# Kernel tuning notes

Measured on AMD Instinct MI355X. Metric: run time of the kernel, lower is better.

The kernel has to match this reference:

```python
import jax, jax.numpy as jnp
import numpy as np

HIDDEN = 1024
NUM_HEADS = 16
HEAD_DIM = HIDDEN // NUM_HEADS


def setup_inputs() -> dict:
    key = jax.random.key(0)
    ks = jax.random.split(key, 5)
    scale = 1.0 / np.sqrt(HIDDEN)
    x = jax.random.normal(ks[0], (2, 2048, HIDDEN), dtype=jnp.float32)
    qkv_w = jax.random.uniform(ks[1], (3 * HIDDEN, HIDDEN), jnp.float32, -scale, scale)
    qkv_b = jax.random.uniform(ks[2], (3 * HIDDEN,), jnp.float32, -scale, scale)
    out_w = jax.random.uniform(ks[3], (HIDDEN, HIDDEN), jnp.float32, -scale, scale)
    out_b = jax.random.uniform(ks[4], (HIDDEN,), jnp.float32, -scale, scale)
    return {"x": x, "qkv_w": qkv_w, "qkv_b": qkv_b, "out_w": out_w, "out_b": out_b}


def reference(x, qkv_w, qkv_b, out_w, out_b):
    B, S, _ = x.shape
    qkv = jnp.einsum('bsd,ed->bse', x, qkv_w) + qkv_b  # [B,S,3H]
    q, k, v = jnp.split(qkv, 3, axis=-1)
    # [B,S,H] -> [B,nh,S,hd]
    def to_heads(t):
        return t.reshape(B, S, NUM_HEADS, HEAD_DIM).transpose(0, 2, 1, 3)
    q, k, v = to_heads(q), to_heads(k), to_heads(v)
    scores = jnp.einsum('bhqd,bhkd->bhqk', q, k) / np.sqrt(HEAD_DIM).astype(np.float32)
    attn = jax.nn.softmax(scores, axis=-1)
    o = jnp.einsum('bhqk,bhkd->bhqd', attn, v)
    o = o.transpose(0, 2, 1, 3).reshape(B, S, HIDDEN)
    return jnp.einsum('bsd,ed->bse', o, out_w) + out_b
```

## Files before the change

### kernel.cpp

```cpp
#include <hip/hip_runtime.h>
#include <stdint.h>

typedef __bf16 bf16x8 __attribute__((ext_vector_type(8)));
typedef float  f32x4  __attribute__((ext_vector_type(4)));
typedef float  f32x16 __attribute__((ext_vector_type(16)));
typedef unsigned short u16;
typedef unsigned int   u32;

#define B_  2
#define S_  2048
#define H_  1024
#define NH_ 16
#define HD_ 64
#define QSCL 0.18033688011112042f

__device__ __forceinline__ u16 f2bf(float f) {
  u32 u = __builtin_bit_cast(u32, f);
  return (u16)((u + 0x7FFFu + ((u >> 16) & 1u)) >> 16);
}
__device__ __forceinline__ float ex2(float x) { return __builtin_amdgcn_exp2f(x); }
__device__ __forceinline__ u32 cvtpk(float lo, float hi) {
  u32 r; asm("v_cvt_pk_bf16_f32 %0, %1, %2" : "=v"(r) : "v"(lo), "v"(hi)); return r;
}
__device__ __forceinline__ void gload_lds16(const u16* g, u16* lds) {
  __builtin_amdgcn_global_load_lds(
      (__attribute__((address_space(1))) void*)(void*)g,
      (__attribute__((address_space(3))) void*)lds, 16, 0, 0);
}

__global__ void cvt_all(const float* __restrict__ a, const float* __restrict__ b,
                        const float* __restrict__ c, u16* __restrict__ oa,
                        u16* __restrict__ ob, u16* __restrict__ oc) {
  int i = blockIdx.x * 256 + threadIdx.x;
  const float4* src; ushort4* dst; int j;
  if (i < 1048576)      { src = (const float4*)a; dst = (ushort4*)oa; j = i; }
  else if (i < 1835008) { src = (const float4*)b; dst = (ushort4*)ob; j = i - 1048576; }
  else                  { src = (const float4*)c; dst = (ushort4*)oc; j = i - 1835008; }
  const float4 v = src[j];
  ushort4 o;
  o.x = f2bf(v.x); o.y = f2bf(v.y); o.z = f2bf(v.z); o.w = f2bf(v.w);
  dst[j] = o;
}

__global__ __launch_bounds__(256, 2)
void gemm_qkv(const u16* __restrict__ A, const u16* __restrict__ W,
              const float* __restrict__ bias,
              u16* __restrict__ qb, u16* __restrict__ kb, u16* __restrict__ vtb,
              int M, int N, int K)
{
  __shared__ __align__(16) u16 As[128 * 32];
  __shared__ __align__(16) u16 Bs[128 * 32];
  const int tid = threadIdx.x;
  const int w = tid >> 6, l = tid & 63;
  const int lg = l >> 4, lr = l & 15;
  const int wr = w >> 1, wc = w & 1;
  const int tM = blockIdx.y * 128, tN = blockIdx.x * 128;

  f32x4 acc[4][4];
  const f32x4 z4 = {0.f, 0.f, 0.f, 0.f};
#pragma unroll
  for (int m = 0; m < 4; ++m)
#pragma unroll
    for (int n = 0; n < 4; ++n) acc[m][n] = z4;

  for (int k0 = 0; k0 < K; k0 += 32) {
    __syncthreads();
#pragma unroll
    for (int i = 0; i < 2; ++i) {
      const int ch = i * 256 + tid;
      const int row = ch >> 2, cc = (ch & 3) * 8;
      gload_lds16(A + (size_t)(tM + row) * K + k0 + cc, As + (size_t)(i * 256 + w * 64) * 8);
      gload_lds16(W + (size_t)(tN + row) * K + k0 + cc, Bs + (size_t)(i * 256 + w * 64) * 8);
    }
    __syncthreads();
    bf16x8 af[4], bw[4];
#pragma unroll
    for (int m = 0; m < 4; ++m)
      af[m] = *(const bf16x8*)&As[(wr * 64 + m * 16 + lr) * 32 + lg * 8];
#pragma unroll
    for (int n = 0; n < 4; ++n)
      bw[n] = *(const bf16x8*)&Bs[(wc * 64 + n * 16 + lr) * 32 + lg * 8];
#pragma unroll
    for (int m = 0; m < 4; ++m)
#pragma unroll
      for (int n = 0; n < 4; ++n)
        acc[m][n] = __builtin_amdgcn_mfma_f32_16x16x32_bf16(af[m], bw[n], acc[m][n], 0, 0, 0);
  }

#pragma unroll
  for (int n = 0; n < 4; ++n) {
    const int col = tN + wc * 64 + n * 16 + lr;
    const float bv = bias[col];
    const int t3 = col >> 10, rem = col & 1023;
    const int hh = rem >> 6, dd = rem & 63;
    const float sc = (t3 == 0) ? QSCL : 1.f;
    u16* dst = (t3 == 0) ? qb : (t3 == 1) ? kb : vtb;
#pragma unroll
    for (int m = 0; m < 4; ++m)
#pragma unroll
      for (int r = 0; r < 4; ++r) {
        const int row = tM + wr * 64 + m * 16 + lg * 4 + r;
        const int bb = row >> 11, ss = row & 2047;
        const u16 val = f2bf((acc[m][n][r] + bv) * sc);
        if (t3 < 2) dst[((size_t)(bb * NH_ + hh) * S_ + ss) * HD_ + dd] = val;
        else        dst[((size_t)(bb * NH_ + hh) * HD_ + dd) * S_ + ss] = val;
      }
  }
}

__global__ __launch_bounds__(256, 2)
void gemm_out(const u16* __restrict__ A, const u16* __restrict__ W,
              const float* __restrict__ bias, float* __restrict__ outf,
              int M, int N, int K)
{
  __shared__ __align__(16) u16 As[128 * 32];
  __shared__ __align__(16) u16 Bs[64 * 32];
  const int tid = threadIdx.x;
  const int w = tid >> 6, l = tid & 63;
  const int lg = l >> 4, lr = l & 15;
  const int tM = blockIdx.y * 128, tN = blockIdx.x * 64;

  f32x4 acc[2][4];
  const f32x4 z4 = {0.f, 0.f, 0.f, 0.f};
#pragma unroll
  for (int m = 0; m < 2; ++m)
#pragma unroll
    for (int n = 0; n < 4; ++n) acc[m][n] = z4;

  for (int k0 = 0; k0 < K; k0 += 32) {
    __syncthreads();
#pragma unroll
    for (int i = 0; i < 2; ++i) {
      const int ch = i * 256 + tid;
      const int row = ch >> 2, cc = (ch & 3) * 8;
      gload_lds16(A + (size_t)(tM + row) * K + k0 + cc, As + (size_t)(i * 256 + w * 64) * 8);
    }
    gload_lds16(W + (size_t)(tN + (tid >> 2)) * K + k0 + (tid & 3) * 8, Bs + (size_t)(w * 64) * 8);
    __syncthreads();
    bf16x8 af[2], bw[4];
#pragma unroll
    for (int m = 0; m < 2; ++m)
      af[m] = *(const bf16x8*)&As[(w * 32 + m * 16 + lr) * 32 + lg * 8];
#pragma unroll
    for (int n = 0; n < 4; ++n)
      bw[n] = *(const bf16x8*)&Bs[(n * 16 + lr) * 32 + lg * 8];
#pragma unroll
    for (int m = 0; m < 2; ++m)
#pragma unroll
      for (int n = 0; n < 4; ++n)
        acc[m][n] = __builtin_amdgcn_mfma_f32_16x16x32_bf16(af[m], bw[n], acc[m][n], 0, 0, 0);
  }

#pragma unroll
  for (int n = 0; n < 4; ++n) {
    const int col = tN + n * 16 + lr;
    const float bv = bias[col];
#pragma unroll
    for (int m = 0; m < 2; ++m)
#pragma unroll
      for (int r = 0; r < 4; ++r) {
        const int row = tM + w * 32 + m * 16 + lg * 4 + r;
        outf[(size_t)row * N + col] = acc[m][n][r] + bv;
      }
  }
}

__global__ __launch_bounds__(256, 2)
void attn_fwd(const u16* __restrict__ qb, const u16* __restrict__ kb,
              const u16* __restrict__ vtb, u16* __restrict__ ob)
{
  __shared__ __align__(16) u16 Kl[2][64 * 64];
  __shared__ __align__(16) u16 Vl[2][64 * 64];

  const int tid = threadIdx.x;
  const int w = tid >> 6, l = tid & 63;
  const int q32 = l & 31, hi = l >> 5;
  const int idx = blockIdx.x;
  const int bh = idx & 31, qt = idx >> 5;
  const int bb = bh >> 4, hh = bh & 15;
  const int q0 = qt * 128 + w * 32;

  bf16x8 qf[4];
#pragma unroll
  for (int ks = 0; ks < 4; ++ks)
    qf[ks] = *(const bf16x8*)&qb[((size_t)bh * S_ + q0 + q32) * HD_ + ks * 16 + hi * 8];

  const f32x16 z16 = {};
  f32x16 acc[2] = {z16, z16};
  float lrun = 0.f;

  const int srow = l >> 3;
  const int scol = ((l & 7) ^ srow) << 3;
  const u16* kbase = kb  + ((size_t)bh * S_  + w * 16 + srow) * HD_ + scol;
  const u16* vbase = vtb + ((size_t)bh * HD_ + w * 16 + srow) * S_  + scol;

  auto STAGE = [&](int buf, int t) {
#pragma unroll
    for (int j = 0; j < 2; ++j) {
      gload_lds16(kbase + (size_t)t * 64 * HD_ + j * 8 * HD_, &Kl[buf][(w * 16 + j * 8) * 64]);
      gload_lds16(vbase + (size_t)t * 64 + j * 8 * S_,        &Vl[buf][(w * 16 + j * 8) * 64]);
    }
  };

  STAGE(0, 0);
  __syncthreads();

  const int sw = q32 & 7;

  for (int t = 0; t < 32; ++t) {
    const int cur = t & 1;
    if (t + 1 < 32) STAGE(cur ^ 1, t + 1);

    f32x16 st[2] = {z16, z16};
    __builtin_amdgcn_s_setprio(1);
#pragma unroll
    for (int kt = 0; kt < 2; ++kt)
#pragma unroll
      for (int ks = 0; ks < 4; ++ks) {
        const bf16x8 kf = *(const bf16x8*)&Kl[cur][(kt * 32 + q32) * 64 + ((((ks << 1) | hi) ^ sw) << 3)];
        st[kt] = __builtin_amdgcn_mfma_f32_32x32x16_bf16(kf, qf[ks], st[kt], 0, 0, 0);
      }
    __builtin_amdgcn_s_setprio(0);

    bf16x8 pa[4];
#pragma unroll
    for (int kt = 0; kt < 2; ++kt) {
      float p[16];
#pragma unroll
      for (int r = 0; r < 16; ++r) p[r] = ex2(st[kt][r]);
#pragma unroll
      for (int g = 0; g < 4; ++g)
        lrun += (p[4 * g] + p[4 * g + 1]) + (p[4 * g + 2] + p[4 * g + 3]);
      u32 wk0[4], wk1[4];
#pragma unroll
      for (int g = 0; g < 4; ++g) {
        wk0[g] = cvtpk(p[4 * g], p[4 * g + 1]);
        wk1[g] = cvtpk(p[4 * g + 2], p[4 * g + 3]);
      }
#pragma unroll
      for (int k2 = 0; k2 < 2; ++k2) {
        u32 a0 = wk0[2 * k2], b0 = wk0[2 * k2 + 1];
        u32 a1 = wk1[2 * k2], b1 = wk1[2 * k2 + 1];
        asm volatile("v_permlane32_swap_b32 %0, %1" : "+v"(a0), "+v"(b0));
        asm volatile("v_permlane32_swap_b32 %0, %1" : "+v"(a1), "+v"(b1));
        uint4 wv = {a0, a1, b0, b1};
        pa[kt * 2 + k2] = __builtin_bit_cast(bf16x8, wv);
      }
    }

    __builtin_amdgcn_s_setprio(1);
#pragma unroll
    for (int dt = 0; dt < 2; ++dt)
#pragma unroll
      for (int ks = 0; ks < 4; ++ks) {
        const bf16x8 vf = *(const bf16x8*)&Vl[cur][(dt * 32 + q32) * 64 + ((((ks << 1) | hi) ^ sw) << 3)];
        acc[dt] = __builtin_amdgcn_mfma_f32_32x32x16_bf16(vf, pa[ks], acc[dt], 0, 0, 0);
      }
    __builtin_amdgcn_s_setprio(0);

    __syncthreads();
  }

  lrun += __shfl_xor(lrun, 32);
  const float linv = 1.f / lrun;
  const size_t orow = ((size_t)(bb * S_ + q0 + q32)) * H_ + hh * HD_;
#pragma unroll
  for (int dt = 0; dt < 2; ++dt)
#pragma unroll
    for (int g = 0; g < 4; ++g) {
      const u32 o0 = cvtpk(acc[dt][4 * g] * linv, acc[dt][4 * g + 1] * linv);
      const u32 o1 = cvtpk(acc[dt][4 * g + 2] * linv, acc[dt][4 * g + 3] * linv);
      uint2 ov; ov.x = o0; ov.y = o1;
      *(uint2*)&ob[orow + dt * 32 + g * 8 + hi * 4] = ov;
    }
}

extern "C" void kernel_launch(void* const* d_in, const int* in_sizes, int n_in,
                              void* d_out, int out_size, void* d_ws, size_t ws_size,
                              hipStream_t stream) {
  const float* x     = (const float*)d_in[0];
  const float* qkv_w = (const float*)d_in[1];
  const float* qkv_b = (const float*)d_in[2];
  const float* out_w = (const float*)d_in[3];
  const float* out_b = (const float*)d_in[4];

  char* ws = (char*)d_ws;
  u16* xb    = (u16*)(ws);
  u16* wqkvb = (u16*)(ws + 8388608);
  u16* wob   = (u16*)(ws + 14680064);
  u16* qb    = (u16*)(ws + 16777216);
  u16* kb    = (u16*)(ws + 25165824);
  u16* vtb   = (u16*)(ws + 33554432);
  u16* ob    = (u16*)(ws + 41943040);

  cvt_all<<<8192, 256, 0, stream>>>(x, qkv_w, out_w, xb, wqkvb, wob);

  gemm_qkv<<<dim3(24, 32), 256, 0, stream>>>(xb, wqkvb, qkv_b,
                                             qb, kb, vtb, 4096, 3072, 1024);
  attn_fwd<<<512, 256, 0, stream>>>(qb, kb, vtb, ob);
  gemm_out<<<dim3(16, 32), 256, 0, stream>>>(ob, wob, out_b, (float*)d_out,
                                             4096, 1024, 1024);
}
```

Baseline: 117.7 us.

## Split attention KV range across wave pairs with LDS reduction of partial outputs

Each block now handles 64 queries instead of 128, and its four waves form two query slices times two KV halves. Each wave processes 32-key tiles over its half of the sequence, and the two partial accumulators and row sums are combined through shared memory at the end. The grid doubles to 1024 blocks and launch bounds target 4 blocks per CU to raise occupancy. The cost is an extra LDS reduction, smaller MFMA batches per iteration, and new swizzle patterns for the narrower K/V tiles.

```diff
diff --git a/kernel.cpp b/kernel.cpp
--- a/kernel.cpp
+++ b/kernel.cpp
@@ -12,6 +12,7 @@
 #define H_  1024
 #define NH_ 16
 #define HD_ 64
+#define KVB 32
 #define QSCL 0.18033688011112042f
 
 __device__ __forceinline__ u16 f2bf(float f) {
@@ -165,20 +166,20 @@
   }
 }
 
-__global__ __launch_bounds__(256, 2)
+__global__ __launch_bounds__(256, 4)
 void attn_fwd(const u16* __restrict__ qb, const u16* __restrict__ kb,
               const u16* __restrict__ vtb, u16* __restrict__ ob)
 {
-  __shared__ __align__(16) u16 Kl[2][64 * 64];
-  __shared__ __align__(16) u16 Vl[2][64 * 64];
+  __shared__ __align__(16) u16 smem[16384];
 
   const int tid = threadIdx.x;
   const int w = tid >> 6, l = tid & 63;
   const int q32 = l & 31, hi = l >> 5;
+  const int qs = w & 1, h = w >> 1;
   const int idx = blockIdx.x;
-  const int bh = idx & 31, qt = idx >> 5;
+  const int bh = idx & 31, qblk = idx >> 5;
   const int bb = bh >> 4, hh = bh & 15;
-  const int q0 = qt * 128 + w * 32;
+  const int q0 = qblk * 64 + qs * 32;
 
   bf16x8 qf[4];
 #pragma unroll
@@ -189,90 +190,131 @@
   f32x16 acc[2] = {z16, z16};
   float lrun = 0.f;
 
-  const int srow = l >> 3;
-  const int scol = ((l & 7) ^ srow) << 3;
-  const u16* kbase = kb  + ((size_t)bh * S_  + w * 16 + srow) * HD_ + scol;
-  const u16* vbase = vtb + ((size_t)bh * HD_ + w * 16 + srow) * S_  + scol;
+  const u16* ksrc0; const u16* ksrc1; const u16* vsrc0; const u16* vsrc1;
+  int kd0, kd1, vd0, vd1;
+  {
+    const int r0 = qs * 16 + (l >> 3), r1 = r0 + 8;
+    const int s0 = (l & 7) ^ (r0 & 7) ^ ((r0 & 16) >> 2);
+    const int s1 = (l & 7) ^ (r1 & 7) ^ ((r1 & 16) >> 2);
+    ksrc0 = kb + ((size_t)bh * S_ + r0) * HD_ + s0 * 8;
+    ksrc1 = kb + ((size_t)bh * S_ + r1) * HD_ + s1 * 8;
+    kd0 = (qs * 16) * 64; kd1 = (qs * 16 + 8) * 64;
+    const int rv0 = qs * 32 + (l >> 2), rv1 = rv0 + 16;
+    const int t0 = (l & 3) ^ ((rv0 >> 1) & 3) ^ ((rv0 & 16) >> 3);
+    const int t1 = (l & 3) ^ ((rv1 >> 1) & 3) ^ ((rv1 & 16) >> 3);
+    vsrc0 = vtb + ((size_t)bh * HD_ + rv0) * S_ + t0 * 8;
+    vsrc1 = vtb + ((size_t)bh * HD_ + rv1) * S_ + t1 * 8;
+    vd0 = (qs * 32) * 32; vd1 = (qs * 32 + 16) * 32;
+  }
+  const int kvbase = h * 1024;
+  const int ktb0 = h * 4096;
+  const int vtb0 = 8192 + h * 4096;
 
   auto STAGE = [&](int buf, int t) {
-#pragma unroll
-    for (int j = 0; j < 2; ++j) {
-      gload_lds16(kbase + (size_t)t * 64 * HD_ + j * 8 * HD_, &Kl[buf][(w * 16 + j * 8) * 64]);
-      gload_lds16(vbase + (size_t)t * 64 + j * 8 * S_,        &Vl[buf][(w * 16 + j * 8) * 64]);
-    }
+    const int kv0 = kvbase + t * KVB;
+    u16* Kt = smem + ktb0 + buf * 2048;
+    u16* Vt = smem + vtb0 + buf * 2048;
+    gload_lds16(ksrc0 + (size_t)kv0 * HD_, Kt + kd0);
+    gload_lds16(ksrc1 + (size_t)kv0 * HD_, Kt + kd1);
+    gload_lds16(vsrc0 + kv0, Vt + vd0);
+    gload_lds16(vsrc1 + kv0, Vt + vd1);
   };
 
   STAGE(0, 0);
   __syncthreads();
 
-  const int sw = q32 & 7;
+  const int rsK = (q32 & 7) ^ ((q32 & 16) >> 2);
+  const int rsV = ((q32 >> 1) & 3) ^ ((q32 & 16) >> 3);
 
   for (int t = 0; t < 32; ++t) {
     const int cur = t & 1;
     if (t + 1 < 32) STAGE(cur ^ 1, t + 1);
-
-    f32x16 st[2] = {z16, z16};
+    const u16* Kt = smem + ktb0 + cur * 2048;
+    const u16* Vt = smem + vtb0 + cur * 2048;
+
+    f32x16 st = z16;
     __builtin_amdgcn_s_setprio(1);
 #pragma unroll
-    for (int kt = 0; kt < 2; ++kt)
-#pragma unroll
-      for (int ks = 0; ks < 4; ++ks) {
-        const bf16x8 kf = *(const bf16x8*)&Kl[cur][(kt * 32 + q32) * 64 + ((((ks << 1) | hi) ^ sw) << 3)];
-        st[kt] = __builtin_amdgcn_mfma_f32_32x32x16_bf16(kf, qf[ks], st[kt], 0, 0, 0);
-      }
+    for (int ks = 0; ks < 4; ++ks) {
+      const bf16x8 kf = *(const bf16x8*)&Kt[q32 * 64 + (((ks * 2 + hi) ^ rsK) << 3)];
+      st = __builtin_amdgcn_mfma_f32_32x32x16_bf16(kf, qf[ks], st, 0, 0, 0);
+    }
     __builtin_amdgcn_s_setprio(0);
 
-    bf16x8 pa[4];
-#pragma unroll
-    for (int kt = 0; kt < 2; ++kt) {
-      float p[16];
-#pragma unroll
-      for (int r = 0; r < 16; ++r) p[r] = ex2(st[kt][r]);
-#pragma unroll
-      for (int g = 0; g < 4; ++g)
-        lrun += (p[4 * g] + p[4 * g + 1]) + (p[4 * g + 2] + p[4 * g + 3]);
-      u32 wk0[4], wk1[4];
+    float p[16];
+#pragma unroll
+    for (int r = 0; r < 16; ++r) p[r] = ex2(st[r]);
+#pragma unroll
+    for (int g = 0; g < 4; ++g)
+      lrun += (p[4 * g] + p[4 * g + 1]) + (p[4 * g + 2] + p[4 * g + 3]);
+    u32 wk0[4], wk1[4];
+#pragma unroll
+    for (int g = 0; g < 4; ++g) {
+      wk0[g] = cvtpk(p[4 * g], p[4 * g + 1]);
+      wk1[g] = cvtpk(p[4 * g + 2], p[4 * g + 3]);
+    }
+    bf16x8 pa[2];
+#pragma unroll
+    for (int k2 = 0; k2 < 2; ++k2) {
+      u32 a0 = wk0[2 * k2], b0 = wk0[2 * k2 + 1];
+      u32 a1 = wk1[2 * k2], b1 = wk1[2 * k2 + 1];
+      asm volatile("v_permlane32_swap_b32 %0, %1" : "+v"(a0), "+v"(b0));
+      asm volatile("v_permlane32_swap_b32 %0, %1" : "+v"(a1), "+v"(b1));
+      uint4 wv = {a0, a1, b0, b1};
+      pa[k2] = __builtin_bit_cast(bf16x8, wv);
+    }
+
+    __builtin_amdgcn_s_setprio(1);
+#pragma unroll
+    for (int dt = 0; dt < 2; ++dt)
+#pragma unroll
+      for (int k2 = 0; k2 < 2; ++k2) {
+        const bf16x8 vf = *(const bf16x8*)&Vt[(dt * 32 + q32) * 32 + (((k2 * 2 + hi) ^ rsV) << 3)];
+        acc[dt] = __builtin_amdgcn_mfma_f32_32x32x16_bf16(vf, pa[k2], acc[dt], 0, 0, 0);
+      }
+    __builtin_amdgcn_s_setprio(0);
+
+    __syncthreads();
+  }
+
+  lrun += __shfl_xor(lrun, 32);
+  __syncthreads();
+  float* slice = (float*)smem + qs * 2112;
+  if (h == 1) {
+#pragma unroll
+    for (int dt = 0; dt < 2; ++dt)
 #pragma unroll
       for (int g = 0; g < 4; ++g) {
-        wk0[g] = cvtpk(p[4 * g], p[4 * g + 1]);
-        wk1[g] = cvtpk(p[4 * g + 2], p[4 * g + 3]);
-      }
-#pragma unroll
-      for (int k2 = 0; k2 < 2; ++k2) {
-        u32 a0 = wk0[2 * k2], b0 = wk0[2 * k2 + 1];
-        u32 a1 = wk1[2 * k2], b1 = wk1[2 * k2 + 1];
-        asm volatile("v_permlane32_swap_b32 %0, %1" : "+v"(a0), "+v"(b0));
-        asm volatile("v_permlane32_swap_b32 %0, %1" : "+v"(a1), "+v"(b1));
-        uint4 wv = {a0, a1, b0, b1};
-        pa[kt * 2 + k2] = __builtin_bit_cast(bf16x8, wv);
-      }
-    }
-
-    __builtin_amdgcn_s_setprio(1);
+        f32x4 v = {acc[dt][4 * g], acc[dt][4 * g + 1], acc[dt][4 * g + 2], acc[dt][4 * g + 3]};
+        *(f32x4*)&slice[q32 * 64 + dt * 32 + g * 8 + hi * 4] = v;
+      }
+    if (hi == 0) slice[2048 + q32] = lrun;
+  }
+  __syncthreads();
+  if (h == 0) {
 #pragma unroll
     for (int dt = 0; dt < 2; ++dt)
 #pragma unroll
-      for (int ks = 0; ks < 4; ++ks) {
-        const bf16x8 vf = *(const bf16x8*)&Vl[cur][(dt * 32 + q32) * 64 + ((((ks << 1) | hi) ^ sw) << 3)];
-        acc[dt] = __builtin_amdgcn_mfma_f32_32x32x16_bf16(vf, pa[ks], acc[dt], 0, 0, 0);
-      }
-    __builtin_amdgcn_s_setprio(0);
-
-    __syncthreads();
-  }
-
-  lrun += __shfl_xor(lrun, 32);
-  const float linv = 1.f / lrun;
-  const size_t orow = ((size_t)(bb * S_ + q0 + q32)) * H_ + hh * HD_;
-#pragma unroll
-  for (int dt = 0; dt < 2; ++dt)
-#pragma unroll
-    for (int g = 0; g < 4; ++g) {
-      const u32 o0 = cvtpk(acc[dt][4 * g] * linv, acc[dt][4 * g + 1] * linv);
-      const u32 o1 = cvtpk(acc[dt][4 * g + 2] * linv, acc[dt][4 * g + 3] * linv);
-      uint2 ov; ov.x = o0; ov.y = o1;
-      *(uint2*)&ob[orow + dt * 32 + g * 8 + hi * 4] = ov;
-    }
+      for (int g = 0; g < 4; ++g) {
+        const f32x4 v = *(const f32x4*)&slice[q32 * 64 + dt * 32 + g * 8 + hi * 4];
+        acc[dt][4 * g]     += v.x;
+        acc[dt][4 * g + 1] += v.y;
+        acc[dt][4 * g + 2] += v.z;
+        acc[dt][4 * g + 3] += v.w;
+      }
+    lrun += slice[2048 + q32];
+    const float linv = 1.f / lrun;
+    const size_t orow = ((size_t)(bb * S_ + q0 + q32)) * H_ + hh * HD_;
+#pragma unroll
+    for (int dt = 0; dt < 2; ++dt)
+#pragma unroll
+      for (int g = 0; g < 4; ++g) {
+        const u32 o0 = cvtpk(acc[dt][4 * g] * linv, acc[dt][4 * g + 1] * linv);
+        const u32 o1 = cvtpk(acc[dt][4 * g + 2] * linv, acc[dt][4 * g + 3] * linv);
+        uint2 ov; ov.x = o0; ov.y = o1;
+        *(uint2*)&ob[orow + dt * 32 + g * 8 + hi * 4] = ov;
+      }
+  }
 }
 
 extern "C" void kernel_launch(void* const* d_in, const int* in_sizes, int n_in,
@@ -297,7 +339,7 @@
 
   gemm_qkv<<<dim3(24, 32), 256, 0, stream>>>(xb, wqkvb, qkv_b,
                                              qb, kb, vtb, 4096, 3072, 1024);
-  attn_fwd<<<512, 256, 0, stream>>>(qb, kb, vtb, ob);
+  attn_fwd<<<1024, 256, 0, stream>>>(qb, kb, vtb, ob);
   gemm_out<<<dim3(16, 32), 256, 0, stream>>>(ob, wob, out_b, (float*)d_out,
                                              4096, 1024, 1024);
 }
```

Result: slower. 120.5 us (+2.4%).

## Double-buffer GEMM LDS tiles and load attention K/V straight into registers

Applied to the files above, without the earlier changes.

Both GEMM kernels now double-buffer their LDS tiles: the next K-slice is staged while the current one feeds the MFMAs, with one barrier per iteration instead of two. The attention kernel drops LDS and barriers entirely. Each wave reads its K and V fragments directly from global memory into registers, with K prefetched one tile ahead in ping-pong register sets. This removes sync and LDS traffic in attention, but each of the four waves now fetches the same K/V separately from global memory or cache and needs more VGPRs. Together that could reduce occupancy or add memory traffic.

```diff
diff --git a/kernel.cpp b/kernel.cpp
--- a/kernel.cpp
+++ b/kernel.cpp
@@ -48,8 +48,8 @@
               u16* __restrict__ qb, u16* __restrict__ kb, u16* __restrict__ vtb,
               int M, int N, int K)
 {
-  __shared__ __align__(16) u16 As[128 * 32];
-  __shared__ __align__(16) u16 Bs[128 * 32];
+  __shared__ __align__(16) u16 As[2][128 * 32];
+  __shared__ __align__(16) u16 Bs[2][128 * 32];
   const int tid = threadIdx.x;
   const int w = tid >> 6, l = tid & 63;
   const int lg = l >> 4, lr = l & 15;
@@ -63,28 +63,35 @@
 #pragma unroll
     for (int n = 0; n < 4; ++n) acc[m][n] = z4;
 
-  for (int k0 = 0; k0 < K; k0 += 32) {
-    __syncthreads();
+  auto STG = [&](int buf, int k0) {
 #pragma unroll
     for (int i = 0; i < 2; ++i) {
       const int ch = i * 256 + tid;
       const int row = ch >> 2, cc = (ch & 3) * 8;
-      gload_lds16(A + (size_t)(tM + row) * K + k0 + cc, As + (size_t)(i * 256 + w * 64) * 8);
-      gload_lds16(W + (size_t)(tN + row) * K + k0 + cc, Bs + (size_t)(i * 256 + w * 64) * 8);
+      gload_lds16(A + (size_t)(tM + row) * K + k0 + cc, As[buf] + (size_t)(i * 256 + w * 64) * 8);
+      gload_lds16(W + (size_t)(tN + row) * K + k0 + cc, Bs[buf] + (size_t)(i * 256 + w * 64) * 8);
     }
-    __syncthreads();
+  };
+
+  STG(0, 0);
+  __syncthreads();
+
+  for (int it = 0; it < K / 32; ++it) {
+    const int cur = it & 1;
+    if (it + 1 < K / 32) STG(cur ^ 1, (it + 1) * 32);
     bf16x8 af[4], bw[4];
 #pragma unroll
     for (int m = 0; m < 4; ++m)
-      af[m] = *(const bf16x8*)&As[(wr * 64 + m * 16 + lr) * 32 + lg * 8];
+      af[m] = *(const bf16x8*)&As[cur][(wr * 64 + m * 16 + lr) * 32 + lg * 8];
 #pragma unroll
     for (int n = 0; n < 4; ++n)
-      bw[n] = *(const bf16x8*)&Bs[(wc * 64 + n * 16 + lr) * 32 + lg * 8];
+      bw[n] = *(const bf16x8*)&Bs[cur][(wc * 64 + n * 16 + lr) * 32 + lg * 8];
 #pragma unroll
     for (int m = 0; m < 4; ++m)
 #pragma unroll
       for (int n = 0; n < 4; ++n)
         acc[m][n] = __builtin_amdgcn_mfma_f32_16x16x32_bf16(af[m], bw[n], acc[m][n], 0, 0, 0);
+    __syncthreads();
   }
 
 #pragma unroll
@@ -113,8 +120,8 @@
               const float* __restrict__ bias, float* __restrict__ outf,
               int M, int N, int K)
 {
-  __shared__ __align__(16) u16 As[128 * 32];
-  __shared__ __align__(16) u16 Bs[64 * 32];
+  __shared__ __align__(16) u16 As[2][128 * 32];
+  __shared__ __align__(16) u16 Bs[2][64 * 32];
   const int tid = threadIdx.x;
   const int w = tid >> 6, l = tid & 63;
   const int lg = l >> 4, lr = l & 15;
@@ -127,28 +134,35 @@
 #pragma unroll
     for (int n = 0; n < 4; ++n) acc[m][n] = z4;
 
-  for (int k0 = 0; k0 < K; k0 += 32) {
-    __syncthreads();
+  auto STG = [&](int buf, int k0) {
 #pragma unroll
     for (int i = 0; i < 2; ++i) {
       const int ch = i * 256 + tid;
       const int row = ch >> 2, cc = (ch & 3) * 8;
-      gload_lds16(A + (size_t)(tM + row) * K + k0 + cc, As + (size_t)(i * 256 + w * 64) * 8);
+      gload_lds16(A + (size_t)(tM + row) * K + k0 + cc, As[buf] + (size_t)(i * 256 + w * 64) * 8);
     }
-    gload_lds16(W + (size_t)(tN + (tid >> 2)) * K + k0 + (tid & 3) * 8, Bs + (size_t)(w * 64) * 8);
-    __syncthreads();
+    gload_lds16(W + (size_t)(tN + (tid >> 2)) * K + k0 + (tid & 3) * 8, Bs[buf] + (size_t)(w * 64) * 8);
+  };
+
+  STG(0, 0);
+  __syncthreads();
+
+  for (int it = 0; it < K / 32; ++it) {
+    const int cur = it & 1;
+    if (it + 1 < K / 32) STG(cur ^ 1, (it + 1) * 32);
     bf16x8 af[2], bw[4];
 #pragma unroll
     for (int m = 0; m < 2; ++m)
-      af[m] = *(const bf16x8*)&As[(w * 32 + m * 16 + lr) * 32 + lg * 8];
+      af[m] = *(const bf16x8*)&As[cur][(w * 32 + m * 16 + lr) * 32 + lg * 8];
 #pragma unroll
     for (int n = 0; n < 4; ++n)
-      bw[n] = *(const bf16x8*)&Bs[(n * 16 + lr) * 32 + lg * 8];
+      bw[n] = *(const bf16x8*)&Bs[cur][(n * 16 + lr) * 32 + lg * 8];
 #pragma unroll
     for (int m = 0; m < 2; ++m)
 #pragma unroll
       for (int n = 0; n < 4; ++n)
         acc[m][n] = __builtin_amdgcn_mfma_f32_16x16x32_bf16(af[m], bw[n], acc[m][n], 0, 0, 0);
+    __syncthreads();
   }
 
 #pragma unroll
@@ -169,9 +183,6 @@
 void attn_fwd(const u16* __restrict__ qb, const u16* __restrict__ kb,
               const u16* __restrict__ vtb, u16* __restrict__ ob)
 {
-  __shared__ __align__(16) u16 Kl[2][64 * 64];
-  __shared__ __align__(16) u16 Vl[2][64 * 64];
-
   const int tid = threadIdx.x;
   const int w = tid >> 6, l = tid & 63;
   const int q32 = l & 31, hi = l >> 5;
@@ -185,81 +196,69 @@
   for (int ks = 0; ks < 4; ++ks)
     qf[ks] = *(const bf16x8*)&qb[((size_t)bh * S_ + q0 + q32) * HD_ + ks * 16 + hi * 8];
 
+  const u16* kfb = kb  + ((size_t)bh * S_  + q32) * HD_ + hi * 8;
+  const u16* vfb = vtb + ((size_t)bh * HD_ + q32) * S_  + hi * 8;
+
   const f32x16 z16 = {};
   f32x16 acc[2] = {z16, z16};
   float lrun = 0.f;
 
-  const int srow = l >> 3;
-  const int scol = ((l & 7) ^ srow) << 3;
-  const u16* kbase = kb  + ((size_t)bh * S_  + w * 16 + srow) * HD_ + scol;
-  const u16* vbase = vtb + ((size_t)bh * HD_ + w * 16 + srow) * S_  + scol;
-
-  auto STAGE = [&](int buf, int t) {
-#pragma unroll
-    for (int j = 0; j < 2; ++j) {
-      gload_lds16(kbase + (size_t)t * 64 * HD_ + j * 8 * HD_, &Kl[buf][(w * 16 + j * 8) * 64]);
-      gload_lds16(vbase + (size_t)t * 64 + j * 8 * S_,        &Vl[buf][(w * 16 + j * 8) * 64]);
-    }
-  };
-
-  STAGE(0, 0);
-  __syncthreads();
-
-  const int sw = q32 & 7;
-
-  for (int t = 0; t < 32; ++t) {
-    const int cur = t & 1;
-    if (t + 1 < 32) STAGE(cur ^ 1, t + 1);
-
-    f32x16 st[2] = {z16, z16};
-    __builtin_amdgcn_s_setprio(1);
-#pragma unroll
-    for (int kt = 0; kt < 2; ++kt)
-#pragma unroll
-      for (int ks = 0; ks < 4; ++ks) {
-        const bf16x8 kf = *(const bf16x8*)&Kl[cur][(kt * 32 + q32) * 64 + ((((ks << 1) | hi) ^ sw) << 3)];
-        st[kt] = __builtin_amdgcn_mfma_f32_32x32x16_bf16(kf, qf[ks], st[kt], 0, 0, 0);
-      }
-    __builtin_amdgcn_s_setprio(0);
-
-    bf16x8 pa[4];
-#pragma unroll
-    for (int kt = 0; kt < 2; ++kt) {
-      float p[16];
-#pragma unroll
-      for (int r = 0; r < 16; ++r) p[r] = ex2(st[kt][r]);
-#pragma unroll
-      for (int g = 0; g < 4; ++g)
-        lrun += (p[4 * g] + p[4 * g + 1]) + (p[4 * g + 2] + p[4 * g + 3]);
-      u32 wk0[4], wk1[4];
-#pragma unroll
-      for (int g = 0; g < 4; ++g) {
-        wk0[g] = cvtpk(p[4 * g], p[4 * g + 1]);
-        wk1[g] = cvtpk(p[4 * g + 2], p[4 * g + 3]);
-      }
-#pragma unroll
-      for (int k2 = 0; k2 < 2; ++k2) {
-        u32 a0 = wk0[2 * k2], b0 = wk0[2 * k2 + 1];
-        u32 a1 = wk1[2 * k2], b1 = wk1[2 * k2 + 1];
-        asm volatile("v_permlane32_swap_b32 %0, %1" : "+v"(a0), "+v"(b0));
-        asm volatile("v_permlane32_swap_b32 %0, %1" : "+v"(a1), "+v"(b1));
-        uint4 wv = {a0, a1, b0, b1};
-        pa[kt * 2 + k2] = __builtin_bit_cast(bf16x8, wv);
-      }
-    }
-
-    __builtin_amdgcn_s_setprio(1);
-#pragma unroll
-    for (int dt = 0; dt < 2; ++dt)
-#pragma unroll
-      for (int ks = 0; ks < 4; ++ks) {
-        const bf16x8 vf = *(const bf16x8*)&Vl[cur][(dt * 32 + q32) * 64 + ((((ks << 1) | hi) ^ sw) << 3)];
-        acc[dt] = __builtin_amdgcn_mfma_f32_32x32x16_bf16(vf, pa[ks], acc[dt], 0, 0, 0);
-      }
-    __builtin_amdgcn_s_setprio(0);
-
-    __syncthreads();
-  }
+  bf16x8 kA[2][4], kB[2][4];
+
+#define LOADK(DST, T)                                                         \
+  { _Pragma("unroll") for (int kt = 0; kt < 2; ++kt)                          \
+    _Pragma("unroll") for (int ks = 0; ks < 4; ++ks)                          \
+      DST[kt][ks] = *(const bf16x8*)(kfb + (size_t)((T) * 64 + kt * 32) * HD_ + ks * 16); }
+
+#define ABODY(KC, KN, TCUR, TNXT)                                             \
+  {                                                                           \
+    bf16x8 vf[2][4];                                                          \
+    _Pragma("unroll") for (int dt = 0; dt < 2; ++dt)                          \
+    _Pragma("unroll") for (int kv = 0; kv < 4; ++kv)                          \
+      vf[dt][kv] = *(const bf16x8*)(vfb + (size_t)dt * 32 * S_ + (TCUR) * 64 + kv * 16); \
+    LOADK(KN, TNXT);                                                          \
+    f32x16 st0 = z16, st1 = z16;                                              \
+    __builtin_amdgcn_s_setprio(1);                                            \
+    _Pragma("unroll") for (int ks = 0; ks < 4; ++ks) {                        \
+      st0 = __builtin_amdgcn_mfma_f32_32x32x16_bf16(KC[0][ks], qf[ks], st0, 0, 0, 0); \
+      st1 = __builtin_amdgcn_mfma_f32_32x32x16_bf16(KC[1][ks], qf[ks], st1, 0, 0, 0); \
+    }                                                                         \
+    __builtin_amdgcn_s_setprio(0);                                            \
+    bf16x8 pa[4];                                                             \
+    _Pragma("unroll") for (int kt = 0; kt < 2; ++kt) {                        \
+      const f32x16 stt = kt ? st1 : st0;                                      \
+      float p[16];                                                            \
+      _Pragma("unroll") for (int r = 0; r < 16; ++r) p[r] = ex2(stt[r]);      \
+      _Pragma("unroll") for (int g = 0; g < 4; ++g)                           \
+        lrun += (p[4 * g] + p[4 * g + 1]) + (p[4 * g + 2] + p[4 * g + 3]);    \
+      u32 wk0[4], wk1[4];                                                     \
+      _Pragma("unroll") for (int g = 0; g < 4; ++g) {                         \
+        wk0[g] = cvtpk(p[4 * g], p[4 * g + 1]);                               \
+        wk1[g] = cvtpk(p[4 * g + 2], p[4 * g + 3]);                           \
+      }                                                                       \
+      _Pragma("unroll") for (int k2 = 0; k2 < 2; ++k2) {                      \
+        u32 a0 = wk0[2 * k2], b0 = wk0[2 * k2 + 1];                           \
+        u32 a1 = wk1[2 * k2], b1 = wk1[2 * k2 + 1];                           \
+        asm volatile("v_permlane32_swap_b32 %0, %1" : "+v"(a0), "+v"(b0));    \
+        asm volatile("v_permlane32_swap_b32 %0, %1" : "+v"(a1), "+v"(b1));    \
+        uint4 wv = {a0, a1, b0, b1};                                          \
+        pa[kt * 2 + k2] = __builtin_bit_cast(bf16x8, wv);                     \
+      }                                                                       \
+    }                                                                         \
+    __builtin_amdgcn_s_setprio(1);                                            \
+    _Pragma("unroll") for (int dt = 0; dt < 2; ++dt)                          \
+    _Pragma("unroll") for (int kv = 0; kv < 4; ++kv)                          \
+      acc[dt] = __builtin_amdgcn_mfma_f32_32x32x16_bf16(vf[dt][kv], pa[kv], acc[dt], 0, 0, 0); \
+    __builtin_amdgcn_s_setprio(0);                                            \
+  }
+
+  LOADK(kA, 0);
+  for (int t = 0; t < 32; t += 2) {
+    ABODY(kA, kB, t, t + 1);
+    ABODY(kB, kA, t + 1, (t + 2 < 32) ? t + 2 : 0);
+  }
+#undef ABODY
+#undef LOADK
 
   lrun += __shfl_xor(lrun, 32);
   const float linv = 1.f / lrun;
```

Result: slower. 189.6 us (+61.1%).

## Double-buffer GEMM LDS tiles and give each attention wave private K/V staging

Applied to the files above, without the earlier changes.

Both GEMM kernels now stage the next K-slice into a second LDS buffer while computing on the current one, which removes one barrier per iteration and overlaps global loads with MFMA work. The attention kernel gives each wave its own K/V buffers in smem with 32-key tiles. Each wave loads its own data, synchronizes with vmcnt waits instead of block barriers, and runs twice as many smaller iterations. This removes cross-wave __syncthreads stalls, but each wave now loads K/V redundantly, which raises global traffic and LDS use (64KB per block), and that may lower occupancy.

```diff
diff --git a/kernel.cpp b/kernel.cpp
--- a/kernel.cpp
+++ b/kernel.cpp
@@ -48,8 +48,8 @@
               u16* __restrict__ qb, u16* __restrict__ kb, u16* __restrict__ vtb,
               int M, int N, int K)
 {
-  __shared__ __align__(16) u16 As[128 * 32];
-  __shared__ __align__(16) u16 Bs[128 * 32];
+  __shared__ __align__(16) u16 As[2][128 * 32];
+  __shared__ __align__(16) u16 Bs[2][128 * 32];
   const int tid = threadIdx.x;
   const int w = tid >> 6, l = tid & 63;
   const int lg = l >> 4, lr = l & 15;
@@ -63,28 +63,35 @@
 #pragma unroll
     for (int n = 0; n < 4; ++n) acc[m][n] = z4;
 
-  for (int k0 = 0; k0 < K; k0 += 32) {
-    __syncthreads();
+  auto STG = [&](int buf, int k0) {
 #pragma unroll
     for (int i = 0; i < 2; ++i) {
       const int ch = i * 256 + tid;
       const int row = ch >> 2, cc = (ch & 3) * 8;
-      gload_lds16(A + (size_t)(tM + row) * K + k0 + cc, As + (size_t)(i * 256 + w * 64) * 8);
-      gload_lds16(W + (size_t)(tN + row) * K + k0 + cc, Bs + (size_t)(i * 256 + w * 64) * 8);
-    }
-    __syncthreads();
+      gload_lds16(A + (size_t)(tM + row) * K + k0 + cc, As[buf] + (size_t)(i * 256 + w * 64) * 8);
+      gload_lds16(W + (size_t)(tN + row) * K + k0 + cc, Bs[buf] + (size_t)(i * 256 + w * 64) * 8);
+    }
+  };
+
+  STG(0, 0);
+  __syncthreads();
+
+  for (int it = 0; it < K / 32; ++it) {
+    const int cur = it & 1;
+    if (it + 1 < K / 32) STG(cur ^ 1, (it + 1) * 32);
     bf16x8 af[4], bw[4];
 #pragma unroll
     for (int m = 0; m < 4; ++m)
-      af[m] = *(const bf16x8*)&As[(wr * 64 + m * 16 + lr) * 32 + lg * 8];
+      af[m] = *(const bf16x8*)&As[cur][(wr * 64 + m * 16 + lr) * 32 + lg * 8];
 #pragma unroll
     for (int n = 0; n < 4; ++n)
-      bw[n] = *(const bf16x8*)&Bs[(wc * 64 + n * 16 + lr) * 32 + lg * 8];
+      bw[n] = *(const bf16x8*)&Bs[cur][(wc * 64 + n * 16 + lr) * 32 + lg * 8];
 #pragma unroll
     for (int m = 0; m < 4; ++m)
 #pragma unroll
       for (int n = 0; n < 4; ++n)
         acc[m][n] = __builtin_amdgcn_mfma_f32_16x16x32_bf16(af[m], bw[n], acc[m][n], 0, 0, 0);
+    __syncthreads();
   }
 
 #pragma unroll
@@ -113,8 +120,8 @@
               const float* __restrict__ bias, float* __restrict__ outf,
               int M, int N, int K)
 {
-  __shared__ __align__(16) u16 As[128 * 32];
-  __shared__ __align__(16) u16 Bs[64 * 32];
+  __shared__ __align__(16) u16 As[2][128 * 32];
+  __shared__ __align__(16) u16 Bs[2][64 * 32];
   const int tid = threadIdx.x;
   const int w = tid >> 6, l = tid & 63;
   const int lg = l >> 4, lr = l & 15;
@@ -127,28 +134,35 @@
 #pragma unroll
     for (int n = 0; n < 4; ++n) acc[m][n] = z4;
 
-  for (int k0 = 0; k0 < K; k0 += 32) {
-    __syncthreads();
+  auto STG = [&](int buf, int k0) {
 #pragma unroll
     for (int i = 0; i < 2; ++i) {
       const int ch = i * 256 + tid;
       const int row = ch >> 2, cc = (ch & 3) * 8;
-      gload_lds16(A + (size_t)(tM + row) * K + k0 + cc, As + (size_t)(i * 256 + w * 64) * 8);
-    }
-    gload_lds16(W + (size_t)(tN + (tid >> 2)) * K + k0 + (tid & 3) * 8, Bs + (size_t)(w * 64) * 8);
-    __syncthreads();
+      gload_lds16(A + (size_t)(tM + row) * K + k0 + cc, As[buf] + (size_t)(i * 256 + w * 64) * 8);
+    }
+    gload_lds16(W + (size_t)(tN + (tid >> 2)) * K + k0 + (tid & 3) * 8, Bs[buf] + (size_t)(w * 64) * 8);
+  };
+
+  STG(0, 0);
+  __syncthreads();
+
+  for (int it = 0; it < K / 32; ++it) {
+    const int cur = it & 1;
+    if (it + 1 < K / 32) STG(cur ^ 1, (it + 1) * 32);
     bf16x8 af[2], bw[4];
 #pragma unroll
     for (int m = 0; m < 2; ++m)
-      af[m] = *(const bf16x8*)&As[(w * 32 + m * 16 + lr) * 32 + lg * 8];
+      af[m] = *(const bf16x8*)&As[cur][(w * 32 + m * 16 + lr) * 32 + lg * 8];
 #pragma unroll
     for (int n = 0; n < 4; ++n)
-      bw[n] = *(const bf16x8*)&Bs[(n * 16 + lr) * 32 + lg * 8];
+      bw[n] = *(const bf16x8*)&Bs[cur][(n * 16 + lr) * 32 + lg * 8];
 #pragma unroll
     for (int m = 0; m < 2; ++m)
 #pragma unroll
       for (int n = 0; n < 4; ++n)
         acc[m][n] = __builtin_amdgcn_mfma_f32_16x16x32_bf16(af[m], bw[n], acc[m][n], 0, 0, 0);
+    __syncthreads();
   }
 
 #pragma unroll
@@ -169,8 +183,7 @@
 void attn_fwd(const u16* __restrict__ qb, const u16* __restrict__ kb,
               const u16* __restrict__ vtb, u16* __restrict__ ob)
 {
-  __shared__ __align__(16) u16 Kl[2][64 * 64];
-  __shared__ __align__(16) u16 Vl[2][64 * 64];
+  __shared__ __align__(16) u16 smem[32768];
 
   const int tid = threadIdx.x;
   const int w = tid >> 6, l = tid & 63;
@@ -180,6 +193,9 @@
   const int bb = bh >> 4, hh = bh & 15;
   const int q0 = qt * 128 + w * 32;
 
+  u16* Kb = smem + w * 8192;
+  u16* Vb = smem + w * 8192 + 4096;
+
   bf16x8 qf[4];
 #pragma unroll
   for (int ks = 0; ks < 4; ++ks)
@@ -189,76 +205,75 @@
   f32x16 acc[2] = {z16, z16};
   float lrun = 0.f;
 
-  const int srow = l >> 3;
-  const int scol = ((l & 7) ^ srow) << 3;
-  const u16* kbase = kb  + ((size_t)bh * S_  + w * 16 + srow) * HD_ + scol;
-  const u16* vbase = vtb + ((size_t)bh * HD_ + w * 16 + srow) * S_  + scol;
+  const u16* ksrcl = kb  + ((size_t)bh * S_  + (l >> 3)) * HD_ + (((l & 7) ^ (l >> 3)) << 3);
+  const u16* vsrcl = vtb + ((size_t)bh * HD_ + (l >> 2)) * S_  + (((l & 3) ^ ((l >> 2) & 3)) << 3);
 
   auto STAGE = [&](int buf, int t) {
 #pragma unroll
-    for (int j = 0; j < 2; ++j) {
-      gload_lds16(kbase + (size_t)t * 64 * HD_ + j * 8 * HD_, &Kl[buf][(w * 16 + j * 8) * 64]);
-      gload_lds16(vbase + (size_t)t * 64 + j * 8 * S_,        &Vl[buf][(w * 16 + j * 8) * 64]);
-    }
+    for (int j = 0; j < 4; ++j)
+      gload_lds16(ksrcl + ((size_t)t * 32 + j * 8) * HD_, Kb + buf * 2048 + j * 512);
+#pragma unroll
+    for (int j = 0; j < 4; ++j)
+      gload_lds16(vsrcl + (size_t)t * 32 + (size_t)j * 16 * S_, Vb + buf * 2048 + j * 512);
   };
 
   STAGE(0, 0);
-  __syncthreads();
-
-  const int sw = q32 & 7;
-
-  for (int t = 0; t < 32; ++t) {
+
+  const int swK = q32 & 7;
+  const int swV = q32 & 3;
+
+  for (int t = 0; t < 64; ++t) {
     const int cur = t & 1;
-    if (t + 1 < 32) STAGE(cur ^ 1, t + 1);
-
-    f32x16 st[2] = {z16, z16};
+    if (t + 1 < 64) {
+      STAGE(cur ^ 1, t + 1);
+      asm volatile("s_waitcnt vmcnt(8)" ::: "memory");
+    } else {
+      asm volatile("s_waitcnt vmcnt(0)" ::: "memory");
+    }
+    const u16* Kt = Kb + cur * 2048;
+    const u16* Vt = Vb + cur * 2048;
+
+    f32x16 st = z16;
     __builtin_amdgcn_s_setprio(1);
 #pragma unroll
-    for (int kt = 0; kt < 2; ++kt)
-#pragma unroll
-      for (int ks = 0; ks < 4; ++ks) {
-        const bf16x8 kf = *(const bf16x8*)&Kl[cur][(kt * 32 + q32) * 64 + ((((ks << 1) | hi) ^ sw) << 3)];
-        st[kt] = __builtin_amdgcn_mfma_f32_32x32x16_bf16(kf, qf[ks], st[kt], 0, 0, 0);
+    for (int ks = 0; ks < 4; ++ks) {
+      const bf16x8 kf = *(const bf16x8*)&Kt[q32 * 64 + (((ks * 2 + hi) ^ swK) << 3)];
+      st = __builtin_amdgcn_mfma_f32_32x32x16_bf16(kf, qf[ks], st, 0, 0, 0);
+    }
+    __builtin_amdgcn_s_setprio(0);
+
+    float p[16];
+#pragma unroll
+    for (int r = 0; r < 16; ++r) p[r] = ex2(st[r]);
+#pragma unroll
+    for (int g = 0; g < 4; ++g)
+      lrun += (p[4 * g] + p[4 * g + 1]) + (p[4 * g + 2] + p[4 * g + 3]);
+    u32 wk0[4], wk1[4];
+#pragma unroll
+    for (int g = 0; g < 4; ++g) {
+      wk0[g] = cvtpk(p[4 * g], p[4 * g + 1]);
+      wk1[g] = cvtpk(p[4 * g + 2], p[4 * g + 3]);
+    }
+    bf16x8 pa[2];
+#pragma unroll
+    for (int k2 = 0; k2 < 2; ++k2) {
+      u32 a0 = wk0[2 * k2], b0 = wk0[2 * k2 + 1];
+      u32 a1 = wk1[2 * k2], b1 = wk1[2 * k2 + 1];
+      asm volatile("v_permlane32_swap_b32 %0, %1" : "+v"(a0), "+v"(b0));
+      asm volatile("v_permlane32_swap_b32 %0, %1" : "+v"(a1), "+v"(b1));
+      uint4 wv = {a0, a1, b0, b1};
+      pa[k2] = __builtin_bit_cast(bf16x8, wv);
+    }
+
+    __builtin_amdgcn_s_setprio(1);
+#pragma unroll
+    for (int dt = 0; dt < 2; ++dt)
+#pragma unroll
+      for (int k2 = 0; k2 < 2; ++k2) {
+        const bf16x8 vf = *(const bf16x8*)&Vt[(dt * 32 + q32) * 32 + (((k2 * 2 + hi) ^ swV) << 3)];
+        acc[dt] = __builtin_amdgcn_mfma_f32_32x32x16_bf16(vf, pa[k2], acc[dt], 0, 0, 0);
       }
     __builtin_amdgcn_s_setprio(0);
-
-    bf16x8 pa[4];
-#pragma unroll
-    for (int kt = 0; kt < 2; ++kt) {
-      float p[16];
-#pragma unroll
-      for (int r = 0; r < 16; ++r) p[r] = ex2(st[kt][r]);
-#pragma unroll
-      for (int g = 0; g < 4; ++g)
-        lrun += (p[4 * g] + p[4 * g + 1]) + (p[4 * g + 2] + p[4 * g + 3]);
-      u32 wk0[4], wk1[4];
-#pragma unroll
-      for (int g = 0; g < 4; ++g) {
-        wk0[g] = cvtpk(p[4 * g], p[4 * g + 1]);
-        wk1[g] = cvtpk(p[4 * g + 2], p[4 * g + 3]);
-      }
-#pragma unroll
-      for (int k2 = 0; k2 < 2; ++k2) {
-        u32 a0 = wk0[2 * k2], b0 = wk0[2 * k2 + 1];
-        u32 a1 = wk1[2 * k2], b1 = wk1[2 * k2 + 1];
-        asm volatile("v_permlane32_swap_b32 %0, %1" : "+v"(a0), "+v"(b0));
-        asm volatile("v_permlane32_swap_b32 %0, %1" : "+v"(a1), "+v"(b1));
-        uint4 wv = {a0, a1, b0, b1};
-        pa[kt * 2 + k2] = __builtin_bit_cast(bf16x8, wv);
-      }
-    }
-
-    __builtin_amdgcn_s_setprio(1);
-#pragma unroll
-    for (int dt = 0; dt < 2; ++dt)
-#pragma unroll
-      for (int ks = 0; ks < 4; ++ks) {
-        const bf16x8 vf = *(const bf16x8*)&Vl[cur][(dt * 32 + q32) * 64 + ((((ks << 1) | hi) ^ sw) << 3)];
-        acc[dt] = __builtin_amdgcn_mfma_f32_32x32x16_bf16(vf, pa[ks], acc[dt], 0, 0, 0);
-      }
-    __builtin_amdgcn_s_setprio(0);
-
-    __syncthreads();
   }
 
   lrun += __shfl_xor(lrun, 32);
```

Result: slower. 122.4 us (+4.0%).
